# Kernel tuning notes

Measured on AMD Instinct MI355X. Metric: run time of the kernel, lower is better.

The kernel has to match this reference:

```python
import jax, jax.numpy as jnp
import numpy as np

# (in_dim, out_dim) for fc1..fc14, hard-coded in the torch module
DIMS = [(12,12),(12,11),(11,10),(10,9),(9,8),(8,7),(7,6),(6,7),(7,8),(8,9),(9,10),(10,11),(11,12),(12,2)]
BATCH = 2_000_000


def setup_inputs() -> dict:
    key = jax.random.key(0)
    keys = jax.random.split(key, 2 * len(DIMS) + 1)
    inp = {"x": jax.random.normal(keys[0], (BATCH, 12), dtype=jnp.float32)}
    for i, (din, dout) in enumerate(DIMS):
        s = 1.0 / np.sqrt(din)  # torch nn.Linear default init range
        inp[f"w{i+1}"] = jax.random.uniform(keys[2*i+1], (dout, din), jnp.float32, -s, s)
        inp[f"b{i+1}"] = jax.random.uniform(keys[2*i+2], (dout,), jnp.float32, -s, s)
    return inp


def _forward(x, Ws, Bs):
    lin = lambda h, i: h @ Ws[i].T + Bs[i]
    # encoder half: fc1..fc6 with ReLU, saving identities 1..6
    ids = []
    h = x
    for i in range(6):
        h = jax.nn.relu(lin(h, i))
        ids.append(h)
    # bottleneck fc7
    h = jax.nn.relu(lin(h, 6))
    # decoder half: fc8..fc13, each adds the matching identity before ReLU
    # fc8 (+id6), fc9 (+id5), ..., fc13 (+id1)
    for i in range(7, 13):
        h = jax.nn.relu(lin(h, i) + ids[12 - i])
    # fc14 + softmax over class dim
    return jax.nn.softmax(lin(h, 13), axis=1)


def reference(x, w1, b1, w2, b2, w3, b3, w4, b4, w5, b5, w6, b6, w7, b7,
              w8, b8, w9, b9, w10, b10, w11, b11, w12, b12, w13, b13, w14, b14):
    Ws = [w1, w2, w3, w4, w5, w6, w7, w8, w9, w10, w11, w12, w13, w14]
    Bs = [b1, b2, b3, b4, b5, b6, b7, b8, b9, b10, b11, b12, b13, b14]
    return _forward(x, Ws, Bs)
```

## Files before the change

### kernel.cpp

```cpp
#include <hip/hip_runtime.h>
#include <math.h>

#define DEV __device__ __forceinline__


typedef _Float16 f16x8 __attribute__((ext_vector_type(8)));
typedef _Float16 h2 __attribute__((ext_vector_type(2)));
typedef float f32x16 __attribute__((ext_vector_type(16)));

union BU { f16x8 v; h2 p[4]; };

DEV h2 pk2(float a, float b) {
    auto t = __builtin_amdgcn_cvt_pkrtz(a, b);
    h2 r;
    __builtin_memcpy(&r, &t, 4);
    return r;
}

DEV h2 bperm(int addr, h2 v) {
    int x;
    __builtin_memcpy(&x, &v, 4);
    int y = __builtin_amdgcn_ds_bpermute(addr, x);
    h2 r;
    __builtin_memcpy(&r, &y, 4);
    return r;
}

DEV f16x8 mk_b(const float* h, bool hi, int xaddr) {
    h2 P01 = pk2(h[0], h[1]);
    h2 P23 = pk2(h[2], h[3]);
    h2 P45 = pk2(h[4], h[5]);
    h2 P67 = pk2(h[6], h[7]);
    h2 sA = hi ? P01 : P45;
    h2 sB = hi ? P23 : P67;
    h2 pA = bperm(xaddr, sA);
    h2 pB = bperm(xaddr, sB);
    const h2 ONES = {(_Float16)1.0f, (_Float16)0.0f};
    const h2 ZER  = {(_Float16)0.0f, (_Float16)0.0f};
    BU u;
    u.p[0] = hi ? pA : P01;
    u.p[1] = hi ? pB : P23;
    u.p[2] = hi ? ONES : pA;
    u.p[3] = hi ? ZER : pB;
    return u.v;
}

struct SrcPtrs { const float* p[28]; };

__global__ void __launch_bounds__(256)
build_a(SrcPtrs ps, f16x8* __restrict__ ws) {
    int t = blockIdx.x * blockDim.x + threadIdx.x;
    if (t >= 14 * 64) return;
    int L = t >> 6, lane = t & 63, m = lane & 31, hi = lane >> 5;
    const int DIN[14]  = {12, 12, 11, 10, 9, 8, 7, 6, 7, 8, 9, 10, 11, 12};
    const int DOUT[14] = {12, 11, 10, 9, 8, 7, 6, 7, 8, 9, 10, 11, 12, 2};
    const float* w = ps.p[2 * L];
    const float* b = ps.p[2 * L + 1];
    f16x8 f;
#pragma unroll
    for (int j = 0; j < 8; ++j) {
        int k = hi * 8 + j;
        float v = 0.0f;
        if (m < DOUT[L]) {
            if (k < DIN[L]) v = w[m * DIN[L] + k];
            else if (k == 12) v = b[m];
        }
        f[j] = (_Float16)v;
    }
    ws[t] = f;
}

#define NTILES 62500

__global__ void __launch_bounds__(256)
csnet14_mfma(const float* __restrict__ x, const f16x8* __restrict__ ws,
             float* __restrict__ out, int nwaves) {
    const int tid  = blockIdx.x * blockDim.x + threadIdx.x;
    const int wave = tid >> 6;
    const int lane = threadIdx.x & 63;
    const int n    = lane & 31;
    const bool hi  = (lane >> 5) != 0;
    const int xadr = (lane ^ 32) * 4;

    f16x8 A[14];
#pragma unroll
    for (int L = 0; L < 14; ++L) A[L] = ws[L * 64 + lane];

    const f32x16 zacc = {};

    for (int tile = wave; tile < NTILES; tile += nwaves) {
        const int b0 = tile * 32;

        const float4* xb = reinterpret_cast<const float4*>(x + (size_t)(b0 + n) * 12);
        float4 a  = xb[hi ? 2 : 0];
        float4 bq = xb[1];
        const h2 ONES = {(_Float16)1.0f, (_Float16)0.0f};
        const h2 ZER  = {(_Float16)0.0f, (_Float16)0.0f};
        BU u;
        u.p[0] = pk2(a.x, a.y);
        u.p[1] = pk2(a.z, a.w);
        u.p[2] = hi ? ONES : pk2(bq.x, bq.y);
        u.p[3] = hi ? ZER  : pk2(bq.z, bq.w);
        f16x8 B = u.v;

        f32x16 C;
        float id1[8], id2[8], id3[8], id4[8], id5[8], id6[8], h[8];

#define ENC(L, IDARR)                                                        \
        C = __builtin_amdgcn_mfma_f32_32x32x16_f16(A[L], B, zacc, 0, 0, 0);  \
        _Pragma("unroll")                                                    \
        for (int r = 0; r < 8; ++r) IDARR[r] = fmaxf(C[r], 0.0f);            \
        B = mk_b(IDARR, hi, xadr);

        ENC(0, id1)
        ENC(1, id2)
        ENC(2, id3)
        ENC(3, id4)
        ENC(4, id5)
        ENC(5, id6)

        C = __builtin_amdgcn_mfma_f32_32x32x16_f16(A[6], B, zacc, 0, 0, 0);
#pragma unroll
        for (int r = 0; r < 8; ++r) h[r] = fmaxf(C[r], 0.0f);
        B = mk_b(h, hi, xadr);

#define DEC(L, IDARR)                                                        \
        C = __builtin_amdgcn_mfma_f32_32x32x16_f16(A[L], B, zacc, 0, 0, 0);  \
        _Pragma("unroll")                                                    \
        for (int r = 0; r < 8; ++r) h[r] = fmaxf(C[r] + IDARR[r], 0.0f);     \
        B = mk_b(h, hi, xadr);

        DEC(7,  id6)
        DEC(8,  id5)
        DEC(9,  id4)
        DEC(10, id3)
        DEC(11, id2)
        DEC(12, id1)

        C = __builtin_amdgcn_mfma_f32_32x32x16_f16(A[13], B, zacc, 0, 0, 0);
        if (!hi) {
            float l0 = C[0], l1 = C[1];
            float mx = fmaxf(l0, l1);
            float e0 = __expf(l0 - mx);
            float e1 = __expf(l1 - mx);
            float inv = __builtin_amdgcn_rcpf(e0 + e1);
            float2 o;
            o.x = e0 * inv;
            o.y = e1 * inv;
            reinterpret_cast<float2*>(out)[b0 + n] = o;
        }
    }
#undef ENC
#undef DEC
}

extern "C" void kernel_launch(void* const* d_in, const int* in_sizes, int n_in,
                              void* d_out, int out_size, void* d_ws, size_t ws_size,
                              hipStream_t stream) {
    const float* x = (const float*)d_in[0];
    float* out = (float*)d_out;
    f16x8* ws = (f16x8*)d_ws;

    SrcPtrs ps;
    for (int i = 0; i < 28; ++i) ps.p[i] = (const float*)d_in[1 + i];

    build_a<<<4, 256, 0, stream>>>(ps, ws);

    const int nblocks = 1024;
    const int nwaves  = nblocks * (256 / 64);
    csnet14_mfma<<<nblocks, 256, 0, stream>>>(x, ws, out, nwaves);
}
```

Baseline: 249.1 us.

## Process two 32-row tiles per wave iteration with packed fp16 activations

Each wave now handles two independent 32-row tiles per loop iteration, interleaving their MFMA chains so one tile's matrix op can overlap the other's ReLU, pack and permute work. Activations and skip identities are stored as packed fp16 pairs, and ReLU and residual adds use packed half ops instead of per-element fp32 max. This should hide MFMA latency and cut VALU and register work, but residual additions now happen in fp16, which may reduce accuracy, and the larger live state could raise register pressure.

```diff
diff --git a/kernel.cpp b/kernel.cpp
--- a/kernel.cpp
+++ b/kernel.cpp
@@ -26,22 +26,30 @@
     return r;
 }
 
-DEV f16x8 mk_b(const float* h, bool hi, int xaddr) {
-    h2 P01 = pk2(h[0], h[1]);
-    h2 P23 = pk2(h[2], h[3]);
-    h2 P45 = pk2(h[4], h[5]);
-    h2 P67 = pk2(h[6], h[7]);
-    h2 sA = hi ? P01 : P45;
-    h2 sB = hi ? P23 : P67;
+DEV h2 h2max0(h2 v) {
+    const h2 Z = {(_Float16)0.0f, (_Float16)0.0f};
+    return __builtin_elementwise_max(v, Z);
+}
+
+DEV void pack4(const f32x16& C, h2 q[4]) {
+    q[0] = pk2(C[0], C[1]);
+    q[1] = pk2(C[2], C[3]);
+    q[2] = pk2(C[4], C[5]);
+    q[3] = pk2(C[6], C[7]);
+}
+
+DEV f16x8 mk_b(const h2 q[4], bool hi, int xaddr) {
+    h2 sA = hi ? q[0] : q[2];
+    h2 sB = hi ? q[1] : q[3];
     h2 pA = bperm(xaddr, sA);
     h2 pB = bperm(xaddr, sB);
     const h2 ONES = {(_Float16)1.0f, (_Float16)0.0f};
     const h2 ZER  = {(_Float16)0.0f, (_Float16)0.0f};
     BU u;
-    u.p[0] = hi ? pA : P01;
-    u.p[1] = hi ? pB : P23;
+    u.p[0] = hi ? pA : q[0];
+    u.p[1] = hi ? pB : q[1];
     u.p[2] = hi ? ONES : pA;
-    u.p[3] = hi ? ZER : pB;
+    u.p[3] = hi ? ZER  : pB;
     return u.v;
 }
 
@@ -70,7 +78,7 @@
     ws[t] = f;
 }
 
-#define NTILES 62500
+#define PAIRS 31250
 
 __global__ void __launch_bounds__(256)
 csnet14_mfma(const float* __restrict__ x, const f16x8* __restrict__ ws,
@@ -88,70 +96,93 @@
 
     const f32x16 zacc = {};
 
-    for (int tile = wave; tile < NTILES; tile += nwaves) {
-        const int b0 = tile * 32;
-
-        const float4* xb = reinterpret_cast<const float4*>(x + (size_t)(b0 + n) * 12);
-        float4 a  = xb[hi ? 2 : 0];
-        float4 bq = xb[1];
-        const h2 ONES = {(_Float16)1.0f, (_Float16)0.0f};
-        const h2 ZER  = {(_Float16)0.0f, (_Float16)0.0f};
-        BU u;
-        u.p[0] = pk2(a.x, a.y);
-        u.p[1] = pk2(a.z, a.w);
-        u.p[2] = hi ? ONES : pk2(bq.x, bq.y);
-        u.p[3] = hi ? ZER  : pk2(bq.z, bq.w);
-        f16x8 B = u.v;
-
-        f32x16 C;
-        float id1[8], id2[8], id3[8], id4[8], id5[8], id6[8], h[8];
-
-#define ENC(L, IDARR)                                                        \
-        C = __builtin_amdgcn_mfma_f32_32x32x16_f16(A[L], B, zacc, 0, 0, 0);  \
-        _Pragma("unroll")                                                    \
-        for (int r = 0; r < 8; ++r) IDARR[r] = fmaxf(C[r], 0.0f);            \
-        B = mk_b(IDARR, hi, xadr);
-
-        ENC(0, id1)
-        ENC(1, id2)
-        ENC(2, id3)
-        ENC(3, id4)
-        ENC(4, id5)
-        ENC(5, id6)
-
-        C = __builtin_amdgcn_mfma_f32_32x32x16_f16(A[6], B, zacc, 0, 0, 0);
-#pragma unroll
-        for (int r = 0; r < 8; ++r) h[r] = fmaxf(C[r], 0.0f);
-        B = mk_b(h, hi, xadr);
-
-#define DEC(L, IDARR)                                                        \
-        C = __builtin_amdgcn_mfma_f32_32x32x16_f16(A[L], B, zacc, 0, 0, 0);  \
-        _Pragma("unroll")                                                    \
-        for (int r = 0; r < 8; ++r) h[r] = fmaxf(C[r] + IDARR[r], 0.0f);     \
-        B = mk_b(h, hi, xadr);
-
-        DEC(7,  id6)
-        DEC(8,  id5)
-        DEC(9,  id4)
-        DEC(10, id3)
-        DEC(11, id2)
-        DEC(12, id1)
-
-        C = __builtin_amdgcn_mfma_f32_32x32x16_f16(A[13], B, zacc, 0, 0, 0);
+    for (int p = wave; p < PAIRS; p += nwaves) {
+        const int base = p * 64;
+
+        f16x8 B[2];
+#pragma unroll
+        for (int c = 0; c < 2; ++c) {
+            const float4* xb =
+                reinterpret_cast<const float4*>(x + (size_t)(base + 32 * c + n) * 12);
+            float4 a  = xb[hi ? 2 : 0];
+            float4 bq = xb[1];
+            const h2 ONES = {(_Float16)1.0f, (_Float16)0.0f};
+            const h2 ZER  = {(_Float16)0.0f, (_Float16)0.0f};
+            BU u;
+            u.p[0] = pk2(a.x, a.y);
+            u.p[1] = pk2(a.z, a.w);
+            u.p[2] = hi ? ONES : pk2(bq.x, bq.y);
+            u.p[3] = hi ? ZER  : pk2(bq.z, bq.w);
+            B[c] = u.v;
+        }
+
+        f32x16 C[2];
+        h2 ids[6][2][4];
+        h2 q[2][4];
+
+#define ENC(L)                                                               \
+        _Pragma("unroll")                                                    \
+        for (int c = 0; c < 2; ++c)                                          \
+            C[c] = __builtin_amdgcn_mfma_f32_32x32x16_f16(A[L], B[c], zacc, 0, 0, 0); \
+        _Pragma("unroll")                                                    \
+        for (int c = 0; c < 2; ++c) {                                        \
+            pack4(C[c], q[c]);                                               \
+            _Pragma("unroll")                                                \
+            for (int j = 0; j < 4; ++j) {                                    \
+                q[c][j] = h2max0(q[c][j]);                                   \
+                ids[L][c][j] = q[c][j];                                      \
+            }                                                                \
+            B[c] = mk_b(q[c], hi, xadr);                                     \
+        }
+
+        ENC(0) ENC(1) ENC(2) ENC(3) ENC(4) ENC(5)
+
+#pragma unroll
+        for (int c = 0; c < 2; ++c)
+            C[c] = __builtin_amdgcn_mfma_f32_32x32x16_f16(A[6], B[c], zacc, 0, 0, 0);
+#pragma unroll
+        for (int c = 0; c < 2; ++c) {
+            pack4(C[c], q[c]);
+#pragma unroll
+            for (int j = 0; j < 4; ++j) q[c][j] = h2max0(q[c][j]);
+            B[c] = mk_b(q[c], hi, xadr);
+        }
+
+#define DEC(L, IDL)                                                          \
+        _Pragma("unroll")                                                    \
+        for (int c = 0; c < 2; ++c)                                          \
+            C[c] = __builtin_amdgcn_mfma_f32_32x32x16_f16(A[L], B[c], zacc, 0, 0, 0); \
+        _Pragma("unroll")                                                    \
+        for (int c = 0; c < 2; ++c) {                                        \
+            pack4(C[c], q[c]);                                               \
+            _Pragma("unroll")                                                \
+            for (int j = 0; j < 4; ++j)                                      \
+                q[c][j] = h2max0(q[c][j] + ids[IDL][c][j]);                  \
+            B[c] = mk_b(q[c], hi, xadr);                                     \
+        }
+
+        DEC(7, 5) DEC(8, 4) DEC(9, 3) DEC(10, 2) DEC(11, 1) DEC(12, 0)
+
+#pragma unroll
+        for (int c = 0; c < 2; ++c)
+            C[c] = __builtin_amdgcn_mfma_f32_32x32x16_f16(A[13], B[c], zacc, 0, 0, 0);
         if (!hi) {
-            float l0 = C[0], l1 = C[1];
-            float mx = fmaxf(l0, l1);
-            float e0 = __expf(l0 - mx);
-            float e1 = __expf(l1 - mx);
-            float inv = __builtin_amdgcn_rcpf(e0 + e1);
-            float2 o;
-            o.x = e0 * inv;
-            o.y = e1 * inv;
-            reinterpret_cast<float2*>(out)[b0 + n] = o;
-        }
-    }
+#pragma unroll
+            for (int c = 0; c < 2; ++c) {
+                float l0 = C[c][0], l1 = C[c][1];
+                float mx = fmaxf(l0, l1);
+                float e0 = __expf(l0 - mx);
+                float e1 = __expf(l1 - mx);
+                float inv = __builtin_amdgcn_rcpf(e0 + e1);
+                float2 o;
+                o.x = e0 * inv;
+                o.y = e1 * inv;
+                reinterpret_cast<float2*>(out)[base + 32 * c + n] = o;
+            }
+        }
 #undef ENC
 #undef DEC
+    }
 }
 
 extern "C" void kernel_launch(void* const* d_in, const int* in_sizes, int n_in,
```

After: 230.9 us. 7.3% less time.
